# Optimization experiments

Measured on AMD Instinct MI355X. Metric: run time of the kernel, lower is better.

Reference implementation:

```python
import jax, jax.numpy as jnp
import numpy as np

FEATURE_DIM = 3072
NUM_HEADS = 3


def setup_inputs() -> dict:
    key = jax.random.key(0)
    ks = jax.random.split(key, 8)
    B = 16384
    D = FEATURE_DIM
    s = 1.0 / np.sqrt(D)  # nn.Linear default init scale
    return {
        "x": jax.random.normal(ks[0], (B, D), dtype=jnp.float32),
        "synthetic_attributes": jax.random.normal(ks[1], (B, D), dtype=jnp.float32),
        "Wq": jax.random.uniform(ks[2], (D, D), dtype=jnp.float32, minval=-s, maxval=s),
        "bq": jax.random.uniform(ks[3], (D,), dtype=jnp.float32, minval=-s, maxval=s),
        "Wk": jax.random.uniform(ks[4], (D, D), dtype=jnp.float32, minval=-s, maxval=s),
        "bk": jax.random.uniform(ks[5], (D,), dtype=jnp.float32, minval=-s, maxval=s),
        "Wv": jax.random.uniform(ks[6], (D, D), dtype=jnp.float32, minval=-s, maxval=s),
        "bv": jax.random.uniform(ks[7], (D,), dtype=jnp.float32, minval=-s, maxval=s),
    }


def reference(x, synthetic_attributes, Wq, bq, Wk, bk, Wv, bv):
    B, D = x.shape
    H = NUM_HEADS
    dh = D // H  # head dim (1024)
    # QKV projections (Linear: y = x @ W^T + b; W stored as [out, in])
    Q = (synthetic_attributes @ Wq.T + bq).reshape(B, H, dh)
    K = (x @ Wk.T + bk).reshape(B, H, dh)
    V = (x @ Wv.T + bv).reshape(B, H, dh)
    # tiny cross-attention: heads act as tokens -> [B, H, H] scores
    scores = jnp.einsum('bhd,bgd->bhg', Q, K) / jnp.sqrt(jnp.float32(dh))
    weights = jax.nn.softmax(scores, axis=-1)
    out = jnp.einsum('bhg,bgd->bhd', weights, V)
    return out.reshape(B, D)
```

## Files before the change

### kernel.cpp

```cpp
#include <hip/hip_runtime.h>
#include <cstdint>
#include <cstddef>


typedef __bf16 bf16x8 __attribute__((ext_vector_type(8)));
typedef float f32x4 __attribute__((ext_vector_type(4)));

#define GLOBAL_AS __attribute__((address_space(1)))
#define LDS_AS __attribute__((address_space(3)))

__device__ __forceinline__ void async_load16(const __bf16* g, __bf16* l) {
    __builtin_amdgcn_global_load_lds((const GLOBAL_AS void*)g, (LDS_AS void*)l,
                                     16, 0, 0);
}

#define DIM 3072
#define BROWS 16384

__global__ __launch_bounds__(256) void cast_f32_bf16(
    const float* __restrict__ src, __bf16* __restrict__ dst, int n8) {
    int i = blockIdx.x * 256 + threadIdx.x;
    if (i >= n8) return;
    const float4* s4 = reinterpret_cast<const float4*>(src);
    float4 a = s4[2 * i];
    float4 b = s4[2 * i + 1];
    bf16x8 o;
    o[0] = (__bf16)a.x; o[1] = (__bf16)a.y; o[2] = (__bf16)a.z; o[3] = (__bf16)a.w;
    o[4] = (__bf16)b.x; o[5] = (__bf16)b.y; o[6] = (__bf16)b.z; o[7] = (__bf16)b.w;
    *reinterpret_cast<bf16x8*>(dst + (size_t)i * 8) = o;
}


#define WAIT8 asm volatile("s_waitcnt vmcnt(8)" ::: "memory");
#define WAIT4 asm volatile("s_waitcnt vmcnt(4)" ::: "memory");
#define WAIT0 asm volatile("s_waitcnt vmcnt(0)" ::: "memory");

#define STAGE_P1(B_, T_) \
    async_load16(agp + (T_) * 32,          &lds[B_][0]     + tid8); \
    async_load16(wgp + (T_) * 32,          &lds[B_][8192]  + tid8);
#define STAGE_P2(B_, T_) \
    async_load16(agp + (T_) * 32 + 393216, &lds[B_][4096]  + tid8); \
    async_load16(wgp + (T_) * 32 + 393216, &lds[B_][12288] + tid8);

#define MFMA16(ACCROW) \
    _Pragma("unroll") \
    for (int mt = 0; mt < 4; ++mt) \
    _Pragma("unroll") \
    for (int nt = 0; nt < 4; ++nt) \
        acc[(ACCROW) + mt][nt] = __builtin_amdgcn_mfma_f32_16x16x32_bf16( \
            af[mt], bfv[nt], acc[(ACCROW) + mt][nt], 0, 0, 0);

#define LOAD_A(B_, EXTRA) \
    _Pragma("unroll") \
    for (int q = 0; q < 4; ++q) \
        af[q] = *reinterpret_cast<const bf16x8*>( \
            &lds[B_][aofs + (EXTRA) + q * 512]);
#define LOAD_B(B_) \
    _Pragma("unroll") \
    for (int q = 0; q < 4; ++q) \
        bfv[q] = *reinterpret_cast<const bf16x8*>( \
            &lds[B_][8192 + bofs + q * 512]);

#define TILE(B_, SB_, T_, W_) { \
    bf16x8 af[4], bfv[4]; \
    LOAD_A(B_, 0) \
    LOAD_B(B_) \
    STAGE_P1(SB_, (T_) + 3) \
    __builtin_amdgcn_s_setprio(1); \
    MFMA16(0) \
    __builtin_amdgcn_s_setprio(0); \
    __builtin_amdgcn_s_barrier(); \
    LOAD_A(B_, 2048) \
    STAGE_P2(SB_, (T_) + 3) \
    __builtin_amdgcn_s_setprio(1); \
    MFMA16(4) \
    __builtin_amdgcn_s_setprio(0); \
    W_ \
    __builtin_amdgcn_s_barrier(); \
}

#define TILE_NS(B_, W_) { \
    bf16x8 af[4], bfv[4]; \
    LOAD_A(B_, 0) \
    LOAD_B(B_) \
    __builtin_amdgcn_s_setprio(1); \
    MFMA16(0) \
    __builtin_amdgcn_s_setprio(0); \
    __builtin_amdgcn_s_barrier(); \
    LOAD_A(B_, 2048) \
    __builtin_amdgcn_s_setprio(1); \
    MFMA16(4) \
    __builtin_amdgcn_s_setprio(0); \
    W_ \
    __builtin_amdgcn_s_barrier(); \
}

#define TILE_LAST(B_) { \
    bf16x8 af[4], bfv[4]; \
    LOAD_A(B_, 0) \
    LOAD_B(B_) \
    MFMA16(0) \
    LOAD_A(B_, 2048) \
    MFMA16(4) \
}

__global__ __launch_bounds__(512, 2) void gemm_qkv(
    const __bf16* __restrict__ xb, const __bf16* __restrict__ sb,
    const __bf16* __restrict__ wqb, const __bf16* __restrict__ wkb,
    const __bf16* __restrict__ wvb,
    const float* __restrict__ bq, const float* __restrict__ bk,
    const float* __restrict__ bv,
    __bf16* __restrict__ qo, __bf16* __restrict__ ko, __bf16* __restrict__ vo) {

    __shared__ __bf16 lds[4][16384];

    const int tid  = threadIdx.x;
    const int lane = tid & 63;
    const int wave = tid >> 6;
    const int wm   = wave >> 2;
    const int wn   = wave & 3;

    const int bid  = blockIdx.x;
    const int swz  = (bid & 7) * 288 + (bid >> 3);
    const int bn   = swz % 36;
    const int bm   = swz / 36;
    const int proj = bn / 12;
    const int n0   = (bn % 12) * 256;
    const int m0   = bm * 256;

    const __bf16* A = (proj == 0) ? sb : xb;
    const __bf16* W = (proj == 0) ? wqb : (proj == 1 ? wkb : wvb);
    const float*  bias = (proj == 0) ? bq : (proj == 1 ? bk : bv);
    __bf16* O = (proj == 0) ? qo : (proj == 1 ? ko : vo);

    const int trow = tid >> 2;
    const int tc   = (tid & 3) ^ ((tid >> 2) & 3) ^ ((tid >> 4) & 3);
    const __bf16* agp = A + (size_t)(m0 + trow) * DIM + tc * 8;
    const __bf16* wgp = W + (size_t)(n0 + trow) * DIM + tc * 8;
    const int tid8 = tid * 8;

    const int lr   = lane & 15;
    const int lc   = lane >> 4;
    const int slot = lc ^ (lr & 3) ^ ((lr >> 2) & 3);
    const int aofs = (wm * 128 + lr) * 32 + slot * 8;
    const int bofs = (wn * 64 + lr) * 32 + slot * 8;

    f32x4 acc[8][4];
#pragma unroll
    for (int mt = 0; mt < 8; ++mt)
#pragma unroll
        for (int nt = 0; nt < 4; ++nt)
            acc[mt][nt] = (f32x4){0.f, 0.f, 0.f, 0.f};

    STAGE_P1(0, 0) STAGE_P2(0, 0)
    STAGE_P1(1, 1) STAGE_P2(1, 1)
    STAGE_P1(2, 2) STAGE_P2(2, 2)
    WAIT8
    __builtin_amdgcn_s_barrier();

    for (int tt = 0; tt < 23; ++tt) {
        const int t = tt * 4;
        TILE(0, 3, t + 0, WAIT8)
        TILE(1, 0, t + 1, WAIT8)
        TILE(2, 1, t + 2, WAIT8)
        TILE(3, 2, t + 3, WAIT8)
    }
    TILE(0, 3, 92, WAIT8)
    TILE_NS(1, WAIT4)
    TILE_NS(2, WAIT0)
    TILE_LAST(3)

    const int lrow4 = (lane >> 4) * 4;
#pragma unroll
    for (int nt = 0; nt < 4; ++nt) {
        const int n = n0 + wn * 64 + nt * 16 + lr;
        const float bn_f = bias[n];
#pragma unroll
        for (int mt = 0; mt < 8; ++mt) {
            const int mbase = m0 + wm * 128 + mt * 16 + lrow4;
#pragma unroll
            for (int r = 0; r < 4; ++r) {
                O[(size_t)(mbase + r) * DIM + n] =
                    (__bf16)(acc[mt][nt][r] + bn_f);
            }
        }
    }
}

__global__ __launch_bounds__(256) void attn_kernel(
    const __bf16* __restrict__ q, const __bf16* __restrict__ k,
    const __bf16* __restrict__ v, float* __restrict__ out) {
    const int wave = threadIdx.x >> 6;
    const int lane = threadIdx.x & 63;
    const size_t b = (size_t)blockIdx.x * 4 + wave;

    const __bf16* qr = q + b * DIM;
    const __bf16* kr = k + b * DIM;
    const __bf16* vr = v + b * DIM;

    float s[3][3] = {{0.f, 0.f, 0.f}, {0.f, 0.f, 0.f}, {0.f, 0.f, 0.f}};

#pragma unroll
    for (int it = 0; it < 2; ++it) {
        const int d0 = it * 512 + lane * 8;
        bf16x8 q8[3], k8[3];
#pragma unroll
        for (int h = 0; h < 3; ++h)
            q8[h] = *reinterpret_cast<const bf16x8*>(qr + h * 1024 + d0);
#pragma unroll
        for (int g = 0; g < 3; ++g)
            k8[g] = *reinterpret_cast<const bf16x8*>(kr + g * 1024 + d0);
#pragma unroll
        for (int h = 0; h < 3; ++h)
#pragma unroll
            for (int g = 0; g < 3; ++g) {
                float acc = 0.f;
#pragma unroll
                for (int j = 0; j < 8; ++j)
                    acc += (float)q8[h][j] * (float)k8[g][j];
                s[h][g] += acc;
            }
    }

#pragma unroll
    for (int h = 0; h < 3; ++h)
#pragma unroll
        for (int g = 0; g < 3; ++g) {
            float val = s[h][g];
#pragma unroll
            for (int off = 32; off > 0; off >>= 1)
                val += __shfl_xor(val, off, 64);
            s[h][g] = val;
        }

    float w[3][3];
    const float scale = 0.03125f;
#pragma unroll
    for (int h = 0; h < 3; ++h) {
        float s0 = s[h][0] * scale, s1 = s[h][1] * scale, s2 = s[h][2] * scale;
        float mx = fmaxf(s0, fmaxf(s1, s2));
        float e0 = __expf(s0 - mx), e1 = __expf(s1 - mx), e2 = __expf(s2 - mx);
        float inv = 1.f / (e0 + e1 + e2);
        w[h][0] = e0 * inv; w[h][1] = e1 * inv; w[h][2] = e2 * inv;
    }

#pragma unroll
    for (int it = 0; it < 2; ++it) {
        const int d0 = it * 512 + lane * 8;
        bf16x8 v8[3];
#pragma unroll
        for (int g = 0; g < 3; ++g)
            v8[g] = *reinterpret_cast<const bf16x8*>(vr + g * 1024 + d0);
#pragma unroll
        for (int h = 0; h < 3; ++h) {
            float o[8];
#pragma unroll
            for (int j = 0; j < 8; ++j)
                o[j] = w[h][0] * (float)v8[0][j] + w[h][1] * (float)v8[1][j] +
                       w[h][2] * (float)v8[2][j];
            float* op = out + b * DIM + h * 1024 + d0;
            float4 lo = {o[0], o[1], o[2], o[3]};
            float4 hi = {o[4], o[5], o[6], o[7]};
            *reinterpret_cast<float4*>(op) = lo;
            *reinterpret_cast<float4*>(op + 4) = hi;
        }
    }
}

extern "C" void kernel_launch(void* const* d_in, const int* in_sizes, int n_in,
                              void* d_out, int out_size, void* d_ws,
                              size_t ws_size, hipStream_t stream) {
    const float* x  = (const float*)d_in[0];
    const float* sa = (const float*)d_in[1];
    const float* Wq = (const float*)d_in[2];
    const float* bq = (const float*)d_in[3];
    const float* Wk = (const float*)d_in[4];
    const float* bk = (const float*)d_in[5];
    const float* Wv = (const float*)d_in[6];
    const float* bv = (const float*)d_in[7];
    float* out = (float*)d_out;

    const size_t B = BROWS, D = DIM;
    __bf16* ws  = (__bf16*)d_ws;
    __bf16* xb  = ws;
    __bf16* sb  = xb + B * D;
    __bf16* wqb = sb + B * D;
    __bf16* wkb = wqb + D * D;
    __bf16* wvb = wkb + D * D;
    __bf16* qo  = wvb + D * D;
    __bf16* ko  = qo + B * D;
    __bf16* vo  = ko + B * D;

    const int nBD8 = (int)(B * D / 8);
    const int nDD8 = (int)(D * D / 8);

    cast_f32_bf16<<<nBD8 / 256, 256, 0, stream>>>(x, xb, nBD8);
    cast_f32_bf16<<<nBD8 / 256, 256, 0, stream>>>(sa, sb, nBD8);
    cast_f32_bf16<<<nDD8 / 256, 256, 0, stream>>>(Wq, wqb, nDD8);
    cast_f32_bf16<<<nDD8 / 256, 256, 0, stream>>>(Wk, wkb, nDD8);
    cast_f32_bf16<<<nDD8 / 256, 256, 0, stream>>>(Wv, wvb, nDD8);

    gemm_qkv<<<2304, 512, 0, stream>>>(xb, sb, wqb, wkb, wvb, bq, bk, bv,
                                       qo, ko, vo);

    attn_kernel<<<BROWS / 4, 256, 0, stream>>>(qo, ko, vo, out);
}
```

Baseline: 1.426 ms.

## Switch GEMM to K=64 double-buffered tiles with finer barrier-phased MFMA schedule

The QKV GEMM mainloop now uses two LDS buffers of 256x64 K-slices instead of four buffers of K=32, with a new 8-chunk XOR swizzle and eight async loads per thread per stage. Each tile is split into four barrier-separated MFMA phases with explicit lgkmcnt waits and priority raising, and the next stage is issued only after the buffer's last read. This halves the number of global-load issue and wait points per K and aims at a tighter interleave of LDS reads with MFMAs, in exchange for a shallower prefetch depth (one tile ahead) and more barriers per tile.

```diff
diff --git a/kernel.cpp b/kernel.cpp
--- a/kernel.cpp
+++ b/kernel.cpp
@@ -31,77 +31,83 @@
 }
 
 
+#define BAR __builtin_amdgcn_s_barrier();
+#define PRIO1 __builtin_amdgcn_s_setprio(1);
+#define PRIO0 __builtin_amdgcn_s_setprio(0);
 #define WAIT8 asm volatile("s_waitcnt vmcnt(8)" ::: "memory");
-#define WAIT4 asm volatile("s_waitcnt vmcnt(4)" ::: "memory");
 #define WAIT0 asm volatile("s_waitcnt vmcnt(0)" ::: "memory");
-
-#define STAGE_P1(B_, T_) \
-    async_load16(agp + (T_) * 32,          &lds[B_][0]     + tid8); \
-    async_load16(wgp + (T_) * 32,          &lds[B_][8192]  + tid8);
-#define STAGE_P2(B_, T_) \
-    async_load16(agp + (T_) * 32 + 393216, &lds[B_][4096]  + tid8); \
-    async_load16(wgp + (T_) * 32 + 393216, &lds[B_][12288] + tid8);
-
-#define MFMA16(ACCROW) \
-    _Pragma("unroll") \
-    for (int mt = 0; mt < 4; ++mt) \
-    _Pragma("unroll") \
-    for (int nt = 0; nt < 4; ++nt) \
-        acc[(ACCROW) + mt][nt] = __builtin_amdgcn_mfma_f32_16x16x32_bf16( \
-            af[mt], bfv[nt], acc[(ACCROW) + mt][nt], 0, 0, 0);
-
-#define LOAD_A(B_, EXTRA) \
+#define LGKM0 asm volatile("s_waitcnt lgkmcnt(0)" ::: "memory"); \
+              __builtin_amdgcn_sched_barrier(0);
+
+#define LOADA(B_, KH, H) \
     _Pragma("unroll") \
     for (int q = 0; q < 4; ++q) \
         af[q] = *reinterpret_cast<const bf16x8*>( \
-            &lds[B_][aofs + (EXTRA) + q * 512]);
-#define LOAD_B(B_) \
+            &lds[B_][aof##KH + (H) * 4096 + q * 1024]);
+#define LOADB(B_, KH) \
     _Pragma("unroll") \
     for (int q = 0; q < 4; ++q) \
         bfv[q] = *reinterpret_cast<const bf16x8*>( \
-            &lds[B_][8192 + bofs + q * 512]);
-
-#define TILE(B_, SB_, T_, W_) { \
+            &lds[B_][bof##KH + q * 1024]);
+
+#define MFMAH(H_) \
+    _Pragma("unroll") \
+    for (int mt = 0; mt < 4; ++mt) \
+    _Pragma("unroll") \
+    for (int nt = 0; nt < 4; ++nt) \
+        acc[(H_) * 4 + mt][nt] = __builtin_amdgcn_mfma_f32_16x16x32_bf16( \
+            af[mt], bfv[nt], acc[(H_) * 4 + mt][nt], 0, 0, 0);
+
+#define STAGE8(B_, OFF) \
+    _Pragma("unroll") \
+    for (int l = 0; l < 4; ++l) \
+        async_load16(aptr[l] + (OFF), &lds[B_][(l * 512 + tid) * 8]); \
+    _Pragma("unroll") \
+    for (int l = 0; l < 4; ++l) \
+        async_load16(wptr[l] + (OFF), &lds[B_][16384 + (l * 512 + tid) * 8]);
+
+#define TILE(B_) { \
     bf16x8 af[4], bfv[4]; \
-    LOAD_A(B_, 0) \
-    LOAD_B(B_) \
-    STAGE_P1(SB_, (T_) + 3) \
-    __builtin_amdgcn_s_setprio(1); \
-    MFMA16(0) \
-    __builtin_amdgcn_s_setprio(0); \
-    __builtin_amdgcn_s_barrier(); \
-    LOAD_A(B_, 2048) \
-    STAGE_P2(SB_, (T_) + 3) \
-    __builtin_amdgcn_s_setprio(1); \
-    MFMA16(4) \
-    __builtin_amdgcn_s_setprio(0); \
-    W_ \
-    __builtin_amdgcn_s_barrier(); \
-}
-
-#define TILE_NS(B_, W_) { \
+    LOADB(B_, 0) LOADA(B_, 0, 0) \
+    BAR LGKM0 \
+    PRIO1 MFMAH(0) PRIO0 BAR \
+    LOADA(B_, 0, 1) \
+    BAR LGKM0 \
+    PRIO1 MFMAH(1) PRIO0 BAR \
+    LOADB(B_, 1) LOADA(B_, 1, 0) \
+    BAR LGKM0 \
+    PRIO1 MFMAH(0) PRIO0 BAR \
+    LOADA(B_, 1, 1) \
+    LGKM0 BAR \
+    STAGE8(B_, kbase) \
+    PRIO1 MFMAH(1) PRIO0 \
+    WAIT8 BAR \
+    kbase += 64; \
+}
+
+#define TILE_NS(B_) { \
     bf16x8 af[4], bfv[4]; \
-    LOAD_A(B_, 0) \
-    LOAD_B(B_) \
-    __builtin_amdgcn_s_setprio(1); \
-    MFMA16(0) \
-    __builtin_amdgcn_s_setprio(0); \
-    __builtin_amdgcn_s_barrier(); \
-    LOAD_A(B_, 2048) \
-    __builtin_amdgcn_s_setprio(1); \
-    MFMA16(4) \
-    __builtin_amdgcn_s_setprio(0); \
-    W_ \
-    __builtin_amdgcn_s_barrier(); \
+    LOADB(B_, 0) LOADA(B_, 0, 0) \
+    BAR LGKM0 \
+    PRIO1 MFMAH(0) PRIO0 BAR \
+    LOADA(B_, 0, 1) \
+    BAR LGKM0 \
+    PRIO1 MFMAH(1) PRIO0 BAR \
+    LOADB(B_, 1) LOADA(B_, 1, 0) \
+    BAR LGKM0 \
+    PRIO1 MFMAH(0) PRIO0 BAR \
+    LOADA(B_, 1, 1) \
+    BAR LGKM0 \
+    PRIO1 MFMAH(1) PRIO0 \
+    WAIT0 BAR \
 }
 
 #define TILE_LAST(B_) { \
     bf16x8 af[4], bfv[4]; \
-    LOAD_A(B_, 0) \
-    LOAD_B(B_) \
-    MFMA16(0) \
-    LOAD_A(B_, 2048) \
-    MFMA16(4) \
+    LOADB(B_, 0) LOADA(B_, 0, 0) MFMAH(0) \
+    LOADA(B_, 0, 1) MFMAH(1) \
+    LOADB(B_, 1) LOADA(B_, 1, 0) MFMAH(0) \
+    LOADA(B_, 1, 1) MFMAH(1) \
 }
 
 __global__ __launch_bounds__(512, 2) void gemm_qkv(
@@ -112,7 +118,7 @@
     const float* __restrict__ bv,
     __bf16* __restrict__ qo, __bf16* __restrict__ ko, __bf16* __restrict__ vo) {
 
-    __shared__ __bf16 lds[4][16384];
+    __shared__ __bf16 lds[2][32768];
 
     const int tid  = threadIdx.x;
     const int lane = tid & 63;
@@ -133,17 +139,23 @@
     const float*  bias = (proj == 0) ? bq : (proj == 1 ? bk : bv);
     __bf16* O = (proj == 0) ? qo : (proj == 1 ? ko : vo);
 
-    const int trow = tid >> 2;
-    const int tc   = (tid & 3) ^ ((tid >> 2) & 3) ^ ((tid >> 4) & 3);
-    const __bf16* agp = A + (size_t)(m0 + trow) * DIM + tc * 8;
-    const __bf16* wgp = W + (size_t)(n0 + trow) * DIM + tc * 8;
-    const int tid8 = tid * 8;
-
-    const int lr   = lane & 15;
-    const int lc   = lane >> 4;
-    const int slot = lc ^ (lr & 3) ^ ((lr >> 2) & 3);
-    const int aofs = (wm * 128 + lr) * 32 + slot * 8;
-    const int bofs = (wn * 64 + lr) * 32 + slot * 8;
+    const int trow8 = tid >> 3;
+    const int gch   = (tid & 7) ^ (trow8 & 7);
+    const __bf16* aptr[4];
+    const __bf16* wptr[4];
+#pragma unroll
+    for (int l = 0; l < 4; ++l) {
+        aptr[l] = A + (size_t)(m0 + l * 64 + trow8) * DIM + gch * 8;
+        wptr[l] = W + (size_t)(n0 + l * 64 + trow8) * DIM + gch * 8;
+    }
+
+    const int lr  = lane & 15;
+    const int lc  = lane >> 4;
+    const int s0  = lc ^ (lr & 7);
+    const int aof0 = (wm * 128 + lr) * 64 + s0 * 8;
+    const int aof1 = (wm * 128 + lr) * 64 + (s0 ^ 4) * 8;
+    const int bof0 = 16384 + (wn * 64 + lr) * 64 + s0 * 8;
+    const int bof1 = 16384 + (wn * 64 + lr) * 64 + (s0 ^ 4) * 8;
 
     f32x4 acc[8][4];
 #pragma unroll
@@ -152,23 +164,19 @@
         for (int nt = 0; nt < 4; ++nt)
             acc[mt][nt] = (f32x4){0.f, 0.f, 0.f, 0.f};
 
-    STAGE_P1(0, 0) STAGE_P2(0, 0)
-    STAGE_P1(1, 1) STAGE_P2(1, 1)
-    STAGE_P1(2, 2) STAGE_P2(2, 2)
+    STAGE8(0, 0)
+    STAGE8(1, 64)
     WAIT8
-    __builtin_amdgcn_s_barrier();
+    BAR
+
+    int kbase = 128;
 
     for (int tt = 0; tt < 23; ++tt) {
-        const int t = tt * 4;
-        TILE(0, 3, t + 0, WAIT8)
-        TILE(1, 0, t + 1, WAIT8)
-        TILE(2, 1, t + 2, WAIT8)
-        TILE(3, 2, t + 3, WAIT8)
-    }
-    TILE(0, 3, 92, WAIT8)
-    TILE_NS(1, WAIT4)
-    TILE_NS(2, WAIT0)
-    TILE_LAST(3)
+        TILE(0)
+        TILE(1)
+    }
+    TILE_NS(0)
+    TILE_LAST(1)
 
     const int lrow4 = (lane >> 4) * 4;
 #pragma unroll
```

Result: slower. 1.508 ms (+5.8%).

## Software-pipeline LDS fragment loads across tiles with new swizzled layout

Applied to the files above, without the earlier changes.

Restructures the GEMM main loop so the A/B fragments of the next LDS buffer are read while the current tile's second MFMA half runs, double-buffering the register fragments (A0/A1, B0/B1) and cutting barriers to one per tile. The global-to-LDS staging is regrouped into A and W halves issued at different points. The LDS layout swizzle changes to a 2-rows-per-64-element scheme aimed at fewer bank conflicts. In exchange it raises register pressure from the extra fragment buffers and tightens the vmcnt wait, which affects how much load latency is hidden.

```diff
diff --git a/kernel.cpp b/kernel.cpp
--- a/kernel.cpp
+++ b/kernel.cpp
@@ -31,77 +31,63 @@
 }
 
 
-#define WAIT8 asm volatile("s_waitcnt vmcnt(8)" ::: "memory");
+#define BAR __builtin_amdgcn_s_barrier();
+#define PRIO1 __builtin_amdgcn_s_setprio(1);
+#define PRIO0 __builtin_amdgcn_s_setprio(0);
 #define WAIT4 asm volatile("s_waitcnt vmcnt(4)" ::: "memory");
 #define WAIT0 asm volatile("s_waitcnt vmcnt(0)" ::: "memory");
 
-#define STAGE_P1(B_, T_) \
-    async_load16(agp + (T_) * 32,          &lds[B_][0]     + tid8); \
-    async_load16(wgp + (T_) * 32,          &lds[B_][8192]  + tid8);
-#define STAGE_P2(B_, T_) \
-    async_load16(agp + (T_) * 32 + 393216, &lds[B_][4096]  + tid8); \
-    async_load16(wgp + (T_) * 32 + 393216, &lds[B_][12288] + tid8);
-
-#define MFMA16(ACCROW) \
+#define LDA(B_, DST, H) \
+    _Pragma("unroll") \
+    for (int q = 0; q < 4; ++q) \
+        DST[q] = *reinterpret_cast<const bf16x8*>( \
+            &lds[B_][aofs + ((H) * 4 + q) * 512]);
+#define LDB(B_, DST) \
+    _Pragma("unroll") \
+    for (int q = 0; q < 4; ++q) \
+        DST[q] = *reinterpret_cast<const bf16x8*>( \
+            &lds[B_][bofs + q * 512]);
+
+#define MFMA16(AF, BF, H) \
     _Pragma("unroll") \
     for (int mt = 0; mt < 4; ++mt) \
     _Pragma("unroll") \
     for (int nt = 0; nt < 4; ++nt) \
-        acc[(ACCROW) + mt][nt] = __builtin_amdgcn_mfma_f32_16x16x32_bf16( \
-            af[mt], bfv[nt], acc[(ACCROW) + mt][nt], 0, 0, 0);
-
-#define LOAD_A(B_, EXTRA) \
-    _Pragma("unroll") \
-    for (int q = 0; q < 4; ++q) \
-        af[q] = *reinterpret_cast<const bf16x8*>( \
-            &lds[B_][aofs + (EXTRA) + q * 512]);
-#define LOAD_B(B_) \
-    _Pragma("unroll") \
-    for (int q = 0; q < 4; ++q) \
-        bfv[q] = *reinterpret_cast<const bf16x8*>( \
-            &lds[B_][8192 + bofs + q * 512]);
-
-#define TILE(B_, SB_, T_, W_) { \
-    bf16x8 af[4], bfv[4]; \
-    LOAD_A(B_, 0) \
-    LOAD_B(B_) \
-    STAGE_P1(SB_, (T_) + 3) \
-    __builtin_amdgcn_s_setprio(1); \
-    MFMA16(0) \
-    __builtin_amdgcn_s_setprio(0); \
-    __builtin_amdgcn_s_barrier(); \
-    LOAD_A(B_, 2048) \
-    STAGE_P2(SB_, (T_) + 3) \
-    __builtin_amdgcn_s_setprio(1); \
-    MFMA16(4) \
-    __builtin_amdgcn_s_setprio(0); \
-    W_ \
-    __builtin_amdgcn_s_barrier(); \
-}
-
-#define TILE_NS(B_, W_) { \
-    bf16x8 af[4], bfv[4]; \
-    LOAD_A(B_, 0) \
-    LOAD_B(B_) \
-    __builtin_amdgcn_s_setprio(1); \
-    MFMA16(0) \
-    __builtin_amdgcn_s_setprio(0); \
-    __builtin_amdgcn_s_barrier(); \
-    LOAD_A(B_, 2048) \
-    __builtin_amdgcn_s_setprio(1); \
-    MFMA16(4) \
-    __builtin_amdgcn_s_setprio(0); \
-    W_ \
-    __builtin_amdgcn_s_barrier(); \
-}
-
-#define TILE_LAST(B_) { \
-    bf16x8 af[4], bfv[4]; \
-    LOAD_A(B_, 0) \
-    LOAD_B(B_) \
-    MFMA16(0) \
-    LOAD_A(B_, 2048) \
-    MFMA16(4) \
+        acc[(H) * 4 + mt][nt] = __builtin_amdgcn_mfma_f32_16x16x32_bf16( \
+            AF[mt], BF[nt], acc[(H) * 4 + mt][nt], 0, 0, 0);
+
+#define STAGE_A(SB_, KB_) \
+    async_load16(aptr0 + (KB_), &lds[SB_][tid8]); \
+    async_load16(aptr1 + (KB_), &lds[SB_][4096 + tid8]);
+#define STAGE_W(SB_, KB_) \
+    async_load16(wptr0 + (KB_), &lds[SB_][8192 + tid8]); \
+    async_load16(wptr1 + (KB_), &lds[SB_][12288 + tid8]);
+
+#define TILE(B_, NB_, SB_, A0, B0C, A1, B1N, WMACRO) { \
+    LDA(B_, A1, 1) \
+    STAGE_A(SB_, kb) \
+    PRIO1 MFMA16(A0, B0C, 0) PRIO0 \
+    LDA(NB_, A0, 0) \
+    LDB(NB_, B1N) \
+    STAGE_W(SB_, kb) \
+    PRIO1 MFMA16(A1, B0C, 1) PRIO0 \
+    WMACRO BAR \
+    kb += 32; \
+}
+
+#define TILE_NS(B_, NB_, A0, B0C, A1, B1N, WMACRO) { \
+    LDA(B_, A1, 1) \
+    PRIO1 MFMA16(A0, B0C, 0) PRIO0 \
+    LDA(NB_, A0, 0) \
+    LDB(NB_, B1N) \
+    PRIO1 MFMA16(A1, B0C, 1) PRIO0 \
+    WMACRO \
+}
+
+#define TILE_LAST(B_, A0, B0C, A1) { \
+    LDA(B_, A1, 1) \
+    MFMA16(A0, B0C, 0) \
+    MFMA16(A1, B0C, 1) \
 }
 
 __global__ __launch_bounds__(512, 2) void gemm_qkv(
@@ -133,17 +119,20 @@
     const float*  bias = (proj == 0) ? bq : (proj == 1 ? bk : bv);
     __bf16* O = (proj == 0) ? qo : (proj == 1 ? ko : vo);
 
-    const int trow = tid >> 2;
-    const int tc   = (tid & 3) ^ ((tid >> 2) & 3) ^ ((tid >> 4) & 3);
-    const __bf16* agp = A + (size_t)(m0 + trow) * DIM + tc * 8;
-    const __bf16* wgp = W + (size_t)(n0 + trow) * DIM + tc * 8;
+    const int p    = (tid & 7) ^ ((tid >> 3) & 7);
+    const int ro   = 2 * (tid >> 3) + (p >> 2);
+    const int co   = (p & 3) * 8;
+    const __bf16* aptr0 = A + (size_t)(m0 + ro) * DIM + co;
+    const __bf16* aptr1 = aptr0 + (size_t)128 * DIM;
+    const __bf16* wptr0 = W + (size_t)(n0 + ro) * DIM + co;
+    const __bf16* wptr1 = wptr0 + (size_t)128 * DIM;
     const int tid8 = tid * 8;
 
-    const int lr   = lane & 15;
-    const int lc   = lane >> 4;
-    const int slot = lc ^ (lr & 3) ^ ((lr >> 2) & 3);
-    const int aofs = (wm * 128 + lr) * 32 + slot * 8;
-    const int bofs = (wn * 64 + lr) * 32 + slot * 8;
+    const int lr  = lane & 15;
+    const int lc  = lane >> 4;
+    const int sA  = (lc + 4 * (lr & 1)) ^ ((lr >> 1) & 7);
+    const int aofs = wm * 4096 + (lr >> 1) * 64 + sA * 8;
+    const int bofs = 8192 + wn * 2048 + (lr >> 1) * 64 + sA * 8;
 
     f32x4 acc[8][4];
 #pragma unroll
@@ -152,23 +141,28 @@
         for (int nt = 0; nt < 4; ++nt)
             acc[mt][nt] = (f32x4){0.f, 0.f, 0.f, 0.f};
 
-    STAGE_P1(0, 0) STAGE_P2(0, 0)
-    STAGE_P1(1, 1) STAGE_P2(1, 1)
-    STAGE_P1(2, 2) STAGE_P2(2, 2)
-    WAIT8
-    __builtin_amdgcn_s_barrier();
+    STAGE_A(0, 0)  STAGE_W(0, 0)
+    STAGE_A(1, 32) STAGE_W(1, 32)
+    STAGE_A(2, 64) STAGE_W(2, 64)
+    WAIT4
+    BAR
+
+    bf16x8 A0[4], A1[4], B0[4], B1[4];
+    LDA(0, A0, 0)
+    LDB(0, B0)
+
+    int kb = 96;
 
     for (int tt = 0; tt < 23; ++tt) {
-        const int t = tt * 4;
-        TILE(0, 3, t + 0, WAIT8)
-        TILE(1, 0, t + 1, WAIT8)
-        TILE(2, 1, t + 2, WAIT8)
-        TILE(3, 2, t + 3, WAIT8)
-    }
-    TILE(0, 3, 92, WAIT8)
-    TILE_NS(1, WAIT4)
-    TILE_NS(2, WAIT0)
-    TILE_LAST(3)
+        TILE(0, 1, 3, A0, B0, A1, B1, WAIT4)
+        TILE(1, 2, 0, A0, B1, A1, B0, WAIT4)
+        TILE(2, 3, 1, A0, B0, A1, B1, WAIT4)
+        TILE(3, 0, 2, A0, B1, A1, B0, WAIT4)
+    }
+    TILE(0, 1, 3, A0, B0, A1, B1, WAIT4)
+    TILE_NS(1, 2, A0, B1, A1, B0, WAIT0 BAR)
+    TILE_NS(2, 3, A0, B0, A1, B1, )
+    TILE_LAST(3, A0, B1, A1)
 
     const int lrow4 = (lane >> 4) * 4;
 #pragma unroll
```

New measurement: 1.418 ms. Within noise of the previous version (-0.5%).
